# Optimization experiments

Measured on AMD Instinct MI355X. Metric: run time of the kernel, lower is better.

Reference implementation:

```python
import jax, jax.numpy as jnp
import numpy as np

N_NODES = 50000


def setup_inputs() -> dict:
    key = jax.random.key(0)
    k1, k2, k3, k4, k5 = jax.random.split(key, 5)
    N, E, F_IN, F_E, F_OUT = N_NODES, 800000, 256, 64, 256
    feat = jax.random.normal(k1, (N, F_IN), dtype=jnp.float32)
    edge_feat = jax.random.normal(k2, (E, F_E), dtype=jnp.float32)
    # glorot-scaled weight for (in_feats+edge_feats, out_feats)
    limit = float(np.sqrt(6.0 / (F_IN + F_E + F_OUT)))
    weight = jax.random.uniform(k3, (F_IN + F_E, F_OUT), minval=-limit, maxval=limit, dtype=jnp.float32)
    bias = jnp.zeros((F_OUT,), dtype=jnp.float32)
    src = jax.random.randint(k4, (E,), 0, N, dtype=jnp.int32)
    dst = jax.random.randint(k5, (E,), 0, N, dtype=jnp.int32)
    return {"feat": feat, "edge_feat": edge_feat, "weight": weight, "bias": bias, "src": src, "dst": dst}


def reference(feat, edge_feat, weight, bias, src, dst):
    N, F_IN = feat.shape
    ones = jnp.ones(src.shape[0], dtype=jnp.float32)
    # out-degree normalization on source features
    out_deg = jax.ops.segment_sum(ones, src, num_segments=N)
    norm_out = jnp.maximum(out_deg, 1.0) ** -0.5  # [N]
    feat_n = feat * norm_out[:, None]
    # message = concat(feat_n[src], edge_feat); sum-aggregate by dst.
    # No activation on messages (double_activation=False), so sum distributes
    # over the concat halves -> two segment sums, identical math.
    agg_h = jax.ops.segment_sum(feat_n[src], dst, num_segments=N)      # [N, F_IN]
    agg_e = jax.ops.segment_sum(edge_feat, dst, num_segments=N)        # [N, F_E]
    rst = jnp.concatenate([agg_h, agg_e], axis=1) @ weight             # [N, F_OUT]
    # in-degree normalization on destination
    in_deg = jax.ops.segment_sum(ones, dst, num_segments=N)
    norm_in = jnp.maximum(in_deg, 1.0) ** -0.5
    rst = rst * norm_in[:, None] + bias
    return jax.nn.relu(rst)
```

## Files before the change

### kernel.cpp

```cpp
#include <hip/hip_runtime.h>

#define FIN 256
#define FE  64
#define FOUT 256
#define KTOT 320

typedef __attribute__((ext_vector_type(8))) short short8;
typedef __attribute__((ext_vector_type(4))) float f32x4;

__device__ inline unsigned short f2bf(float f) {
    unsigned int u = __builtin_bit_cast(unsigned int, f);
    u += 0x7fffu + ((u >> 16) & 1u);
    return (unsigned short)(u >> 16);
}
__device__ inline float bfu(unsigned short b) {
    return __builtin_bit_cast(float, (unsigned int)b << 16);
}


__global__ void k_deg_prepw(const int* __restrict__ src, const int* __restrict__ dst,
                            int* __restrict__ out_deg, int* __restrict__ in_deg,
                            const float* __restrict__ w, unsigned short* __restrict__ wtt,
                            int E) {
    int i = blockIdx.x * blockDim.x + threadIdx.x;
    if (i < E) {
        atomicAdd(&out_deg[src[i]], 1);
        atomicAdd(&in_deg[dst[i]], 1);
    }
    if (i < KTOT * 256) {
        int k = i >> 8, n = i & 255;
        wtt[n * KTOT + k] = f2bf(w[i]);
    }
}


__global__ __launch_bounds__(1024) void k_scan(const int* __restrict__ in_deg,
                                               const int* __restrict__ out_deg,
                                               int* __restrict__ row_ptr,
                                               int* __restrict__ cursor,
                                               float* __restrict__ norm_out,
                                               float* __restrict__ norm_in, int N) {
    __shared__ int red[16];
    __shared__ int wsum[16];
    __shared__ int wo[17];
    int b = blockIdx.x, t = threadIdx.x;
    int lane = t & 63, w = t >> 6;
    int limit = b << 10;

    int part = 0;
    for (int i = t; i < limit; i += 1024) part += in_deg[i];
#pragma unroll
    for (int off = 32; off; off >>= 1) part += __shfl_down(part, off, 64);
    if (lane == 0) red[w] = part;
    __syncthreads();
    if (t == 0) {
        int s = 0;
#pragma unroll
        for (int k = 0; k < 16; k++) s += red[k];
        red[0] = s;
    }
    __syncthreads();
    int base = red[0];

    int i = limit + t;
    int v = (i < N) ? in_deg[i] : 0;
    int incl = v;
#pragma unroll
    for (int off = 1; off < 64; off <<= 1) {
        int x = __shfl_up(incl, off, 64);
        if (lane >= off) incl += x;
    }
    if (lane == 63) wsum[w] = incl;
    __syncthreads();
    if (w == 0 && lane < 16) {
        int s = wsum[lane];
        int sc = s;
#pragma unroll
        for (int off = 1; off < 16; off <<= 1) {
            int x = __shfl_up(sc, off, 64);
            if (lane >= off) sc += x;
        }
        wo[lane] = sc - s;
        if (lane == 15) wo[16] = sc;
    }
    __syncthreads();
    int excl = base + wo[w] + incl - v;
    if (i < N) {
        row_ptr[i] = excl;
        cursor[i] = excl;
        norm_in[i]  = 1.0f / sqrtf((float)max(v, 1));
        norm_out[i] = 1.0f / sqrtf((float)max(out_deg[i], 1));
    }
    if (t == 0 && i + 1024 > N && i < N + 1024) row_ptr[N] = base + wo[16];
}


__global__ void k_scatter_prepf(const int* __restrict__ src, const int* __restrict__ dst,
                                int* __restrict__ cursor, int2* __restrict__ s_se, int E,
                                const float* __restrict__ feat,
                                const float* __restrict__ norm_out,
                                unsigned short* __restrict__ featb, int N) {
    int i = blockIdx.x * blockDim.x + threadIdx.x;
    if (i < E) {
        int d = dst[i];
        int p = atomicAdd(&cursor[d], 1);
        s_se[p] = make_int2(src[i], i);
    }
    if (i < N * 64) {
        int m = i >> 6, c4 = (i & 63) * 4;
        float s = norm_out[m];
        float4 v = *(const float4*)&feat[(size_t)m * FIN + c4];
        ushort4 o;
        o.x = f2bf(v.x * s); o.y = f2bf(v.y * s); o.z = f2bf(v.z * s); o.w = f2bf(v.w * s);
        *(ushort4*)&featb[(size_t)m * FIN + c4] = o;
    }
}


#define GTM  32
#define AKLD 328

__global__ __launch_bounds__(512) void k_agg_gemm(const unsigned short* __restrict__ featb,
                                                  const float* __restrict__ edge_feat,
                                                  const int* __restrict__ row_ptr,
                                                  const int2* __restrict__ s_se,
                                                  const unsigned short* __restrict__ Wt,
                                                  const float* __restrict__ norm_in,
                                                  const float* __restrict__ bias,
                                                  float* __restrict__ out, int N) {
    __shared__ unsigned short As[GTM * AKLD];
    int t = threadIdx.x;
    int w = t >> 6, lane = t & 63;
    int quad = lane >> 4, l16 = lane & 15;
    int m0 = blockIdx.x * GTM;

#pragma unroll 1
    for (int i = 0; i < 4; i++) {
        int row = w * 4 + i;
        int n = m0 + row;
        float h0 = 0.f, h1 = 0.f, h2 = 0.f, h3 = 0.f, eacc = 0.f;
        if (n < N) {
            int beg = row_ptr[n], end = row_ptr[n + 1];
            int p = beg;
            for (; p + 8 <= end; p += 8) {
                int2 i0 = s_se[p + 0], i1 = s_se[p + 1], i2 = s_se[p + 2], i3 = s_se[p + 3];
                int2 i4 = s_se[p + 4], i5 = s_se[p + 5], i6 = s_se[p + 6], i7 = s_se[p + 7];
                ushort4 f0 = *(const ushort4*)&featb[(size_t)i0.x * FIN + lane * 4];
                ushort4 f1 = *(const ushort4*)&featb[(size_t)i1.x * FIN + lane * 4];
                ushort4 f2 = *(const ushort4*)&featb[(size_t)i2.x * FIN + lane * 4];
                ushort4 f3 = *(const ushort4*)&featb[(size_t)i3.x * FIN + lane * 4];
                ushort4 f4 = *(const ushort4*)&featb[(size_t)i4.x * FIN + lane * 4];
                ushort4 f5 = *(const ushort4*)&featb[(size_t)i5.x * FIN + lane * 4];
                ushort4 f6 = *(const ushort4*)&featb[(size_t)i6.x * FIN + lane * 4];
                ushort4 f7 = *(const ushort4*)&featb[(size_t)i7.x * FIN + lane * 4];
                float e0 = __builtin_nontemporal_load(&edge_feat[(size_t)i0.y * FE + lane]);
                float e1 = __builtin_nontemporal_load(&edge_feat[(size_t)i1.y * FE + lane]);
                float e2 = __builtin_nontemporal_load(&edge_feat[(size_t)i2.y * FE + lane]);
                float e3 = __builtin_nontemporal_load(&edge_feat[(size_t)i3.y * FE + lane]);
                float e4 = __builtin_nontemporal_load(&edge_feat[(size_t)i4.y * FE + lane]);
                float e5 = __builtin_nontemporal_load(&edge_feat[(size_t)i5.y * FE + lane]);
                float e6 = __builtin_nontemporal_load(&edge_feat[(size_t)i6.y * FE + lane]);
                float e7 = __builtin_nontemporal_load(&edge_feat[(size_t)i7.y * FE + lane]);
                h0 += ((bfu(f0.x) + bfu(f1.x)) + (bfu(f2.x) + bfu(f3.x))) +
                      ((bfu(f4.x) + bfu(f5.x)) + (bfu(f6.x) + bfu(f7.x)));
                h1 += ((bfu(f0.y) + bfu(f1.y)) + (bfu(f2.y) + bfu(f3.y))) +
                      ((bfu(f4.y) + bfu(f5.y)) + (bfu(f6.y) + bfu(f7.y)));
                h2 += ((bfu(f0.z) + bfu(f1.z)) + (bfu(f2.z) + bfu(f3.z))) +
                      ((bfu(f4.z) + bfu(f5.z)) + (bfu(f6.z) + bfu(f7.z)));
                h3 += ((bfu(f0.w) + bfu(f1.w)) + (bfu(f2.w) + bfu(f3.w))) +
                      ((bfu(f4.w) + bfu(f5.w)) + (bfu(f6.w) + bfu(f7.w)));
                eacc += ((e0 + e1) + (e2 + e3)) + ((e4 + e5) + (e6 + e7));
            }
            if (p + 4 <= end) {
                int2 i0 = s_se[p + 0], i1 = s_se[p + 1], i2 = s_se[p + 2], i3 = s_se[p + 3];
                ushort4 f0 = *(const ushort4*)&featb[(size_t)i0.x * FIN + lane * 4];
                ushort4 f1 = *(const ushort4*)&featb[(size_t)i1.x * FIN + lane * 4];
                ushort4 f2 = *(const ushort4*)&featb[(size_t)i2.x * FIN + lane * 4];
                ushort4 f3 = *(const ushort4*)&featb[(size_t)i3.x * FIN + lane * 4];
                float e0 = __builtin_nontemporal_load(&edge_feat[(size_t)i0.y * FE + lane]);
                float e1 = __builtin_nontemporal_load(&edge_feat[(size_t)i1.y * FE + lane]);
                float e2 = __builtin_nontemporal_load(&edge_feat[(size_t)i2.y * FE + lane]);
                float e3 = __builtin_nontemporal_load(&edge_feat[(size_t)i3.y * FE + lane]);
                h0 += (bfu(f0.x) + bfu(f1.x)) + (bfu(f2.x) + bfu(f3.x));
                h1 += (bfu(f0.y) + bfu(f1.y)) + (bfu(f2.y) + bfu(f3.y));
                h2 += (bfu(f0.z) + bfu(f1.z)) + (bfu(f2.z) + bfu(f3.z));
                h3 += (bfu(f0.w) + bfu(f1.w)) + (bfu(f2.w) + bfu(f3.w));
                eacc += (e0 + e1) + (e2 + e3);
                p += 4;
            }
            for (; p < end; p++) {
                int2 a = s_se[p];
                ushort4 f0 = *(const ushort4*)&featb[(size_t)a.x * FIN + lane * 4];
                h0 += bfu(f0.x); h1 += bfu(f0.y); h2 += bfu(f0.z); h3 += bfu(f0.w);
                eacc += __builtin_nontemporal_load(&edge_feat[(size_t)a.y * FE + lane]);
            }
        }
        ushort4 o;
        o.x = f2bf(h0); o.y = f2bf(h1); o.z = f2bf(h2); o.w = f2bf(h3);
        *(ushort4*)&As[row * AKLD + lane * 4] = o;
        As[row * AKLD + FIN + lane] = f2bf(eacc);
    }
    __syncthreads();

    f32x4 acc[2][2];
#pragma unroll
    for (int i = 0; i < 2; i++)
#pragma unroll
        for (int j = 0; j < 2; j++) acc[i][j] = (f32x4){0.f, 0.f, 0.f, 0.f};

    const unsigned short* pW = Wt + (size_t)(w * 32 + l16) * KTOT + quad * 8;

    for (int k0 = 0; k0 < KTOT; k0 += 64) {
#pragma unroll
        for (int kk = 0; kk < 2; kk++) {
            short8 af[2], bf2[2];
#pragma unroll
            for (int i = 0; i < 2; i++)
                af[i] = *(const short8*)&As[(i * 16 + l16) * AKLD + k0 + kk * 32 + quad * 8];
#pragma unroll
            for (int j = 0; j < 2; j++)
                bf2[j] = *(const short8*)&pW[(size_t)(j * 16) * KTOT + k0 + kk * 32];
#pragma unroll
            for (int i = 0; i < 2; i++)
#pragma unroll
                for (int j = 0; j < 2; j++)
                    acc[i][j] = __builtin_amdgcn_mfma_f32_16x16x32_bf16(af[i], bf2[j], acc[i][j], 0, 0, 0);
        }
    }

#pragma unroll
    for (int i = 0; i < 2; i++)
#pragma unroll
        for (int r = 0; r < 4; r++) {
            int gm = m0 + i * 16 + quad * 4 + r;
            if (gm < N) {
                float ni = norm_in[gm];
#pragma unroll
                for (int j = 0; j < 2; j++) {
                    int gn = w * 32 + j * 16 + l16;
                    float v = fmaxf(acc[i][j][r] * ni + bias[gn], 0.f);
                    __builtin_nontemporal_store(v, &out[(size_t)gm * FOUT + gn]);
                }
            }
        }
}


extern "C" void kernel_launch(void* const* d_in, const int* in_sizes, int n_in,
                              void* d_out, int out_size, void* d_ws, size_t ws_size,
                              hipStream_t stream) {
    const float* feat      = (const float*)d_in[0];
    const float* edge_feat = (const float*)d_in[1];
    const float* weight    = (const float*)d_in[2];
    const float* bias      = (const float*)d_in[3];
    const int*   src       = (const int*)d_in[4];
    const int*   dst       = (const int*)d_in[5];
    int E = in_sizes[4];
    int N = in_sizes[0] / FIN;

    char* ws = (char*)d_ws;
    size_t off = 0;
    auto alloc = [&](size_t bytes) -> void* {
        void* p = ws + off;
        off += (bytes + 255) & ~(size_t)255;
        return p;
    };
    unsigned short* featb = (unsigned short*)alloc((size_t)N * FIN * 2);
    unsigned short* wtt   = (unsigned short*)alloc((size_t)256 * KTOT * 2);
    int*   out_deg  = (int*)alloc((size_t)2 * N * 4);
    int*   in_deg   = out_deg + N;
    int*   row_ptr  = (int*)alloc((size_t)(N + 1) * 4);
    int*   cursor   = (int*)alloc((size_t)N * 4);
    float* norm_out = (float*)alloc((size_t)N * 4);
    float* norm_in  = (float*)alloc((size_t)N * 4);
    int2*  s_se     = (int2*)alloc((size_t)E * 8);
    (void)ws_size;

    int bE = (E + 255) / 256;
    int nchunk = (N + 1023) >> 10;

    hipMemsetAsync(out_deg, 0, (size_t)2 * N * 4, stream);

    k_deg_prepw<<<bE, 256, 0, stream>>>(src, dst, out_deg, in_deg, weight, wtt, E);
    k_scan<<<nchunk, 1024, 0, stream>>>(in_deg, out_deg, row_ptr, cursor,
                                        norm_out, norm_in, N);
    k_scatter_prepf<<<(N * 64 + 255) / 256, 256, 0, stream>>>(src, dst, cursor, s_se, E,
                                                              feat, norm_out, featb, N);

    k_agg_gemm<<<(N + GTM - 1) / GTM, 512, 0, stream>>>(featb, edge_feat, row_ptr, s_se,
                                                        wtt, norm_in, bias,
                                                        (float*)d_out, N);
}
```

Baseline: 522.4 us.

## Preload edge indices per wave with lane loads and double-buffer gather chunks

Each wave now reads all five row_ptr entries up front and loads up to 64 (src, edge) index pairs per row with one coalesced lane-parallel load. Lanes then share those indices by shuffle instead of every lane loading s_se. Gathers run in chunks of four edges with two register buffers, so the next chunk's feature and edge loads are in flight while the current chunk is summed. This targets index-load latency and serialized gather latency, at the cost of more registers, shuffles and per-element branches, plus a scalar fallback loop for rows with more than 64 edges.

```diff
diff --git a/kernel.cpp b/kernel.cpp
--- a/kernel.cpp
+++ b/kernel.cpp
@@ -119,6 +119,26 @@
 
 #define GTM  32
 #define AKLD 328
+
+#define ISSUE_G(FB, EB, c0, IV, CNT)                                              \
+    _Pragma("unroll") for (int k = 0; k < 4; k++) {                               \
+        int j = (c0) * 4 + k;                                                     \
+        if (j < (CNT)) {                                                          \
+            int sx = __shfl((IV).x, j), sy = __shfl((IV).y, j);                   \
+            FB[k] = *(const ushort4*)&featb[(size_t)sx * FIN + lane * 4];         \
+            EB[k] = __builtin_nontemporal_load(&edge_feat[(size_t)sy * FE + lane]); \
+        }                                                                         \
+    }
+
+#define ACCUM_G(FB, EB, c0, CNT)                                                  \
+    _Pragma("unroll") for (int k = 0; k < 4; k++) {                               \
+        int j = (c0) * 4 + k;                                                     \
+        if (j < (CNT)) {                                                          \
+            h0 += bfu(FB[k].x); h1 += bfu(FB[k].y);                               \
+            h2 += bfu(FB[k].z); h3 += bfu(FB[k].w);                               \
+            eacc += EB[k];                                                        \
+        }                                                                         \
+    }
 
 __global__ __launch_bounds__(512) void k_agg_gemm(const unsigned short* __restrict__ featb,
                                                   const float* __restrict__ edge_feat,
@@ -134,67 +154,46 @@
     int quad = lane >> 4, l16 = lane & 15;
     int m0 = blockIdx.x * GTM;
 
-#pragma unroll 1
-    for (int i = 0; i < 4; i++) {
-        int row = w * 4 + i;
-        int n = m0 + row;
+    int n0 = m0 + w * 4;
+
+    int rpl[5];
+#pragma unroll
+    for (int q = 0; q < 5; q++) rpl[q] = row_ptr[min(n0 + q, N)];
+
+    int2 iv[4];
+#pragma unroll
+    for (int q = 0; q < 4; q++) {
+        int d = min(rpl[q + 1] - rpl[q], 64);
+        iv[q] = make_int2(0, 0);
+        if (lane < d) iv[q] = s_se[rpl[q] + lane];
+    }
+
+#pragma unroll
+    for (int q = 0; q < 4; q++) {
+        int beg = rpl[q], end = rpl[q + 1];
+        int cnt = min(end - beg, 64);
         float h0 = 0.f, h1 = 0.f, h2 = 0.f, h3 = 0.f, eacc = 0.f;
-        if (n < N) {
-            int beg = row_ptr[n], end = row_ptr[n + 1];
-            int p = beg;
-            for (; p + 8 <= end; p += 8) {
-                int2 i0 = s_se[p + 0], i1 = s_se[p + 1], i2 = s_se[p + 2], i3 = s_se[p + 3];
-                int2 i4 = s_se[p + 4], i5 = s_se[p + 5], i6 = s_se[p + 6], i7 = s_se[p + 7];
-                ushort4 f0 = *(const ushort4*)&featb[(size_t)i0.x * FIN + lane * 4];
-                ushort4 f1 = *(const ushort4*)&featb[(size_t)i1.x * FIN + lane * 4];
-                ushort4 f2 = *(const ushort4*)&featb[(size_t)i2.x * FIN + lane * 4];
-                ushort4 f3 = *(const ushort4*)&featb[(size_t)i3.x * FIN + lane * 4];
-                ushort4 f4 = *(const ushort4*)&featb[(size_t)i4.x * FIN + lane * 4];
-                ushort4 f5 = *(const ushort4*)&featb[(size_t)i5.x * FIN + lane * 4];
-                ushort4 f6 = *(const ushort4*)&featb[(size_t)i6.x * FIN + lane * 4];
-                ushort4 f7 = *(const ushort4*)&featb[(size_t)i7.x * FIN + lane * 4];
-                float e0 = __builtin_nontemporal_load(&edge_feat[(size_t)i0.y * FE + lane]);
-                float e1 = __builtin_nontemporal_load(&edge_feat[(size_t)i1.y * FE + lane]);
-                float e2 = __builtin_nontemporal_load(&edge_feat[(size_t)i2.y * FE + lane]);
-                float e3 = __builtin_nontemporal_load(&edge_feat[(size_t)i3.y * FE + lane]);
-                float e4 = __builtin_nontemporal_load(&edge_feat[(size_t)i4.y * FE + lane]);
-                float e5 = __builtin_nontemporal_load(&edge_feat[(size_t)i5.y * FE + lane]);
-                float e6 = __builtin_nontemporal_load(&edge_feat[(size_t)i6.y * FE + lane]);
-                float e7 = __builtin_nontemporal_load(&edge_feat[(size_t)i7.y * FE + lane]);
-                h0 += ((bfu(f0.x) + bfu(f1.x)) + (bfu(f2.x) + bfu(f3.x))) +
-                      ((bfu(f4.x) + bfu(f5.x)) + (bfu(f6.x) + bfu(f7.x)));
-                h1 += ((bfu(f0.y) + bfu(f1.y)) + (bfu(f2.y) + bfu(f3.y))) +
-                      ((bfu(f4.y) + bfu(f5.y)) + (bfu(f6.y) + bfu(f7.y)));
-                h2 += ((bfu(f0.z) + bfu(f1.z)) + (bfu(f2.z) + bfu(f3.z))) +
-                      ((bfu(f4.z) + bfu(f5.z)) + (bfu(f6.z) + bfu(f7.z)));
-                h3 += ((bfu(f0.w) + bfu(f1.w)) + (bfu(f2.w) + bfu(f3.w))) +
-                      ((bfu(f4.w) + bfu(f5.w)) + (bfu(f6.w) + bfu(f7.w)));
-                eacc += ((e0 + e1) + (e2 + e3)) + ((e4 + e5) + (e6 + e7));
+
+        int nch = (cnt + 3) >> 2;
+        ushort4 fbA[4], fbB[4];
+        float   ebA[4], ebB[4];
+        if (nch > 0) {
+            ISSUE_G(fbA, ebA, 0, iv[q], cnt);
+            for (int c = 0; c < nch; c += 2) {
+                if (c + 1 < nch) ISSUE_G(fbB, ebB, c + 1, iv[q], cnt);
+                ACCUM_G(fbA, ebA, c, cnt);
+                if (c + 2 < nch) ISSUE_G(fbA, ebA, c + 2, iv[q], cnt);
+                if (c + 1 < nch) ACCUM_G(fbB, ebB, c + 1, cnt);
             }
-            if (p + 4 <= end) {
-                int2 i0 = s_se[p + 0], i1 = s_se[p + 1], i2 = s_se[p + 2], i3 = s_se[p + 3];
-                ushort4 f0 = *(const ushort4*)&featb[(size_t)i0.x * FIN + lane * 4];
-                ushort4 f1 = *(const ushort4*)&featb[(size_t)i1.x * FIN + lane * 4];
-                ushort4 f2 = *(const ushort4*)&featb[(size_t)i2.x * FIN + lane * 4];
-                ushort4 f3 = *(const ushort4*)&featb[(size_t)i3.x * FIN + lane * 4];
-                float e0 = __builtin_nontemporal_load(&edge_feat[(size_t)i0.y * FE + lane]);
-                float e1 = __builtin_nontemporal_load(&edge_feat[(size_t)i1.y * FE + lane]);
-                float e2 = __builtin_nontemporal_load(&edge_feat[(size_t)i2.y * FE + lane]);
-                float e3 = __builtin_nontemporal_load(&edge_feat[(size_t)i3.y * FE + lane]);
-                h0 += (bfu(f0.x) + bfu(f1.x)) + (bfu(f2.x) + bfu(f3.x));
-                h1 += (bfu(f0.y) + bfu(f1.y)) + (bfu(f2.y) + bfu(f3.y));
-                h2 += (bfu(f0.z) + bfu(f1.z)) + (bfu(f2.z) + bfu(f3.z));
-                h3 += (bfu(f0.w) + bfu(f1.w)) + (bfu(f2.w) + bfu(f3.w));
-                eacc += (e0 + e1) + (e2 + e3);
-                p += 4;
-            }
-            for (; p < end; p++) {
-                int2 a = s_se[p];
-                ushort4 f0 = *(const ushort4*)&featb[(size_t)a.x * FIN + lane * 4];
-                h0 += bfu(f0.x); h1 += bfu(f0.y); h2 += bfu(f0.z); h3 += bfu(f0.w);
-                eacc += __builtin_nontemporal_load(&edge_feat[(size_t)a.y * FE + lane]);
-            }
-        }
+        }
+        for (int p = beg + 64; p < end; p++) {
+            int2 a = s_se[p];
+            ushort4 f0 = *(const ushort4*)&featb[(size_t)a.x * FIN + lane * 4];
+            h0 += bfu(f0.x); h1 += bfu(f0.y); h2 += bfu(f0.z); h3 += bfu(f0.w);
+            eacc += __builtin_nontemporal_load(&edge_feat[(size_t)a.y * FE + lane]);
+        }
+
+        int row = w * 4 + q;
         ushort4 o;
         o.x = f2bf(h0); o.y = f2bf(h1); o.z = f2bf(h2); o.w = f2bf(h3);
         *(ushort4*)&As[row * AKLD + lane * 4] = o;
```

After: 524.4 us. Within noise of the previous version (+0.4%).
